# Optimization experiments

Measured on AMD Instinct MI355X. Metric: run time of the kernel, lower is better.

## Reference

```python
import jax, jax.numpy as jnp
import numpy as np


def gcn_conv(x, edge_index, edge_weight, W, b):
    """PyG-style GCNConv: h = x @ W; add self-loops (w=1); sym deg^-1/2 norm;
    scatter-add aggregation; + bias."""
    N = x.shape[0]
    h = x @ W                                   # [N, F_out]
    row, col = edge_index[0], edge_index[1]     # src, dst
    loop = jnp.arange(N)
    row = jnp.concatenate([row, loop])
    col = jnp.concatenate([col, loop])
    ew = jnp.concatenate([edge_weight, jnp.ones((N,), edge_weight.dtype)])
    deg = jax.ops.segment_sum(ew, col, num_segments=N)
    dinv = jnp.where(deg > 0, deg ** -0.5, 0.0)
    norm = dinv[row] * ew * dinv[col]           # [E+N]
    out = jax.ops.segment_sum(h[row] * norm[:, None], col, num_segments=N)
    return out + b


def setup_inputs() -> dict:
    key = jax.random.key(0)
    ks = jax.random.split(key, 12)
    N, F_in, H, O, E = 20000, 3000, 512, 256, 640000
    x = jax.random.normal(ks[0], (N, F_in), dtype=jnp.float32)
    sim_edge_index = jax.random.randint(ks[1], (2, E), 0, N, dtype=jnp.int64)
    sim_edge_weight = jax.random.uniform(ks[2], (E,), dtype=jnp.float32)
    dist_edge_index = jax.random.randint(ks[3], (2, E), 0, N, dtype=jnp.int64)
    dist_edge_weight = jax.random.uniform(ks[4], (E,), dtype=jnp.float32)
    s = 0.02
    return {
        "x": x,
        "sim_edge_index": sim_edge_index,
        "sim_edge_weight": sim_edge_weight,
        "dist_edge_index": dist_edge_index,
        "dist_edge_weight": dist_edge_weight,
        "W1": jax.random.normal(ks[5], (F_in, H), dtype=jnp.float32) * s,
        "b1": jnp.zeros((H,), jnp.float32),
        "W2": jax.random.normal(ks[6], (F_in, H), dtype=jnp.float32) * s,
        "b2": jnp.zeros((H,), jnp.float32),
        "Ws": jax.random.normal(ks[7], (H, O), dtype=jnp.float32) * s,
        "bs": jnp.zeros((O,), jnp.float32),
        "Wd": jax.random.normal(ks[8], (H, O), dtype=jnp.float32) * s,
        "bd": jnp.zeros((O,), jnp.float32),
        "Wf": jax.random.normal(ks[9], (2 * O, O), dtype=jnp.float32) * s,
        "bf": jnp.zeros((O,), jnp.float32),
    }


def reference(x, sim_edge_index, sim_edge_weight, dist_edge_index,
              dist_edge_weight, W1, b1, W2, b2, Ws, bs, Wd, bd, Wf, bf):
    # eval mode: dropout is identity
    xs = jax.nn.relu(gcn_conv(x, sim_edge_index, sim_edge_weight, W1, b1))
    xd = jax.nn.relu(gcn_conv(x, dist_edge_index, dist_edge_weight, W2, b2))
    x_sim = gcn_conv(xs, sim_edge_index, sim_edge_weight, Ws, bs)
    x_dist = gcn_conv(xd, dist_edge_index, dist_edge_weight, Wd, bd)
    fused = jnp.concatenate([x_sim, x_dist], axis=1) @ Wf + bf
    return (x_sim, x_dist, fused)
```

## Files before the change

kernel.cpp:

```cpp
#include <hip/hip_runtime.h>
#include <cstdint>
#include <cstddef>

typedef unsigned short u16;
typedef __bf16 bf16x8 __attribute__((ext_vector_type(8)));
typedef float f32x4 __attribute__((ext_vector_type(4)));

#define N_NODES 20000
#define MPAD    20096
#define E_EDGES 640000
#define K1      3000
#define K1P     3008
#define H_DIM   512
#define NW      1024
#define O_DIM   256

__device__ __forceinline__ float bf2f(unsigned int hi) {
  union { unsigned int u; float f; } v; v.u = hi << 16; return v.f;
}
__device__ __forceinline__ u16 f2bf(float f) {
  union { float f; unsigned int u; } v; v.f = f;
  unsigned int u = v.u;
  return (u16)((u + 0x7fffu + ((u >> 16) & 1u)) >> 16);
}

__device__ __forceinline__ void gl2lds16(const void* g, void* l) {
  __builtin_amdgcn_global_load_lds((const __attribute__((address_space(1))) void*)g,
                                   (__attribute__((address_space(3))) void*)l, 16, 0, 0);
}

__global__ __launch_bounds__(256) void deg_init_k(float* degS, float* degD, int* cntS, int* cntD) {
  int i = blockIdx.x * 256 + threadIdx.x;
  if (i < N_NODES) { degS[i] = 1.0f; degD[i] = 1.0f; cntS[i] = 0; cntD[i] = 0; }
}

__global__ __launch_bounds__(256) void deg_accum_k(const int* eiS, const float* ewS,
                                                   const int* eiD, const float* ewD,
                                                   float* degS, float* degD, int* cntS, int* cntD) {
  int e = blockIdx.x * 256 + threadIdx.x;
  if (e < E_EDGES) {
    int cs = eiS[E_EDGES + e];
    atomicAdd(&degS[cs], ewS[e]);
    atomicAdd(&cntS[cs], 1);
    int cd = eiD[E_EDGES + e];
    atomicAdd(&degD[cd], ewD[e]);
    atomicAdd(&cntD[cd], 1);
  }
}

__global__ __launch_bounds__(256) void dinv_k(const float* degS, const float* degD,
                                              float* dinvS, float* dinvD) {
  int i = blockIdx.x * 256 + threadIdx.x;
  if (i < N_NODES) { dinvS[i] = rsqrtf(degS[i]); dinvD[i] = rsqrtf(degD[i]); }
}

__global__ __launch_bounds__(1024) void scan_k(const int* cntS, int* offS, int* curS,
                                               const int* cntD, int* offD, int* curD) {
  const int* cnt = blockIdx.x ? cntD : cntS;
  int* off = blockIdx.x ? offD : offS;
  int* cur = blockIdx.x ? curD : curS;
  __shared__ int sums[1024];
  const int t = threadIdx.x;
  const int CH = 20;
  int base = t * CH;
  int s = 0;
  for (int j = 0; j < CH; ++j) { int idx = base + j; if (idx < N_NODES) s += cnt[idx]; }
  sums[t] = s;
  __syncthreads();
  for (int d = 1; d < 1024; d <<= 1) {
    int v = (t >= d) ? sums[t - d] : 0;
    __syncthreads();
    sums[t] += v;
    __syncthreads();
  }
  int run = sums[t] - s;
  for (int j = 0; j < CH; ++j) {
    int idx = base + j;
    if (idx <= N_NODES) {
      off[idx] = run; cur[idx] = run;
      if (idx < N_NODES) run += cnt[idx];
    }
  }
}

__global__ __launch_bounds__(256) void scatter_k(const int* eiS, const float* ewS, const float* dinvS,
                                                 int* curS, int* ssrcS, float* snrmS,
                                                 const int* eiD, const float* ewD, const float* dinvD,
                                                 int* curD, int* ssrcD, float* snrmD) {
  int e = blockIdx.x * 256 + threadIdx.x;
  if (e < E_EDGES) {
    {
      int r = eiS[e], c = eiS[E_EDGES + e];
      int pos = atomicAdd(&curS[c], 1);
      ssrcS[pos] = r;
      snrmS[pos] = dinvS[r] * ewS[e] * dinvS[c];
    }
    {
      int r = eiD[e], c = eiD[E_EDGES + e];
      int pos = atomicAdd(&curD[c], 1);
      ssrcD[pos] = r;
      snrmD[pos] = dinvD[r] * ewD[e] * dinvD[c];
    }
  }
}

__global__ __launch_bounds__(256) void conv_x_k(const float* __restrict__ x, u16* __restrict__ xb) {
  const int row = blockIdx.x;
  for (int c = threadIdx.x; c < 376; c += 256) {
    uint4 o = {0, 0, 0, 0};
    if (row < N_NODES && c < 375) {
      const float4* p = (const float4*)(x + (size_t)row * K1 + (size_t)c * 8);
      float4 v0 = p[0], v1 = p[1];
      o.x = f2bf(v0.x) | ((unsigned)f2bf(v0.y) << 16);
      o.y = f2bf(v0.z) | ((unsigned)f2bf(v0.w) << 16);
      o.z = f2bf(v1.x) | ((unsigned)f2bf(v1.y) << 16);
      o.w = f2bf(v1.z) | ((unsigned)f2bf(v1.w) << 16);
    }
    *(uint4*)(xb + (size_t)row * K1P + (size_t)c * 8) = o;
  }
}

__global__ __launch_bounds__(256) void conv_w12_k(const float* __restrict__ W1,
                                                  const float* __restrict__ W2,
                                                  u16* __restrict__ w12t) {
  __shared__ float t[64][65];
  const int kb = blockIdx.x;
  const int nb = blockIdx.y;
  const int n0 = nb * 64;
  const float* W = (n0 < H_DIM) ? W1 : W2;
  const int nn0 = n0 & (H_DIM - 1);
  const int k0 = kb * 64;
  const int tc = threadIdx.x & 63;
  const int tr4 = threadIdx.x >> 6;
#pragma unroll
  for (int rr = 0; rr < 16; ++rr) {
    int r = tr4 * 16 + rr;
    int k = k0 + r;
    t[r][tc] = (k < K1) ? W[(size_t)k * H_DIM + nn0 + tc] : 0.f;
  }
  __syncthreads();
#pragma unroll
  for (int rr = 0; rr < 16; ++rr) {
    int n = tr4 * 16 + rr;
    w12t[(size_t)(n0 + n) * K1P + k0 + tc] = f2bf(t[tc][n]);
  }
}

__global__ __launch_bounds__(256) void conv_wsm_k(const float* Ws, const float* Wd, const float* Wf,
                                                  u16* wst, u16* wdt, u16* wft) {
  __shared__ float t[64][65];
  const int which = blockIdx.z;
  const float* W = (which == 0) ? Ws : (which == 1) ? Wd : Wf;
  u16* o = (which == 0) ? wst : (which == 1) ? wdt : wft;
  const int k0 = blockIdx.x * 64;
  const int n0 = blockIdx.y * 64;
  const int tc = threadIdx.x & 63;
  const int tr4 = threadIdx.x >> 6;
#pragma unroll
  for (int rr = 0; rr < 16; ++rr) {
    int r = tr4 * 16 + rr;
    t[r][tc] = W[(size_t)(k0 + r) * O_DIM + n0 + tc];
  }
  __syncthreads();
#pragma unroll
  for (int rr = 0; rr < 16; ++rr) {
    int n = tr4 * 16 + rr;
    o[(size_t)(n0 + n) * H_DIM + k0 + tc] = f2bf(t[tc][n]);
  }
}

template <typename CT, bool BIAS>
__global__ __launch_bounds__(256) void gemm_bt(const u16* __restrict__ A, const u16* __restrict__ Bt,
                                               CT* __restrict__ C, const float* __restrict__ bias,
                                               int Mreal, int K, int ldc) {
  __shared__ alignas(16) u16 As[128 * 64];
  __shared__ alignas(16) u16 Bs[128 * 64];
  const int tid = threadIdx.x;
  const int lane = tid & 63;
  const int wv = tid >> 6;
  const int bm = blockIdx.y * 128;
  const int bn = blockIdx.x * 128;

  const int wm = (wv >> 1) << 6;
  const int wn = (wv & 1) << 6;
  const int frow = lane & 15;
  const int q = lane >> 4;
  const int r7 = lane & 7;

  const int srow = tid >> 3;
  const int sgr = ((tid & 7) ^ ((tid >> 3) & 7)) << 3;
  const u16* ga = A + (size_t)(bm + srow) * K + sgr;
  const u16* gb = Bt + (size_t)(bn + srow) * K + sgr;
  u16* la = &As[wv * 512];
  u16* lb = &Bs[wv * 512];

  f32x4 acc[4][4] = {};

  for (int k0 = 0; k0 < K; k0 += 64) {
#pragma unroll
    for (int r = 0; r < 4; ++r) {
      gl2lds16(ga + (size_t)(r * 32) * K + k0, la + r * 2048);
      gl2lds16(gb + (size_t)(r * 32) * K + k0, lb + r * 2048);
    }
    __syncthreads();
#pragma unroll
    for (int ks = 0; ks < 64; ks += 32) {
      const int p = (((q + (ks >> 3)) ^ r7) << 3);
      bf16x8 af[4], bv[4];
#pragma unroll
      for (int t = 0; t < 4; ++t) {
        af[t] = *(const bf16x8*)&As[(wm + t * 16 + frow) * 64 + p];
        bv[t] = *(const bf16x8*)&Bs[(wn + t * 16 + frow) * 64 + p];
      }
#pragma unroll
      for (int i = 0; i < 4; ++i)
#pragma unroll
        for (int j = 0; j < 4; ++j)
          acc[i][j] = __builtin_amdgcn_mfma_f32_16x16x32_bf16(af[i], bv[j], acc[i][j], 0, 0, 0);
    }
    __syncthreads();
  }

  const int crow = (lane >> 4) << 2;
  const int ccol = lane & 15;
#pragma unroll
  for (int i = 0; i < 4; ++i) {
#pragma unroll
    for (int r = 0; r < 4; ++r) {
      int gr = bm + wm + i * 16 + crow + r;
      if (gr < Mreal) {
#pragma unroll
        for (int j = 0; j < 4; ++j) {
          int gc = bn + wn + j * 16 + ccol;
          float v = acc[i][j][r];
          if constexpr (BIAS) v += bias[gc];
          if constexpr (sizeof(CT) == 2) C[(size_t)gr * ldc + gc] = (CT)f2bf(v);
          else C[(size_t)gr * ldc + gc] = (CT)v;
        }
      }
    }
  }
}

__global__ __launch_bounds__(256) void agg1_k(const u16* __restrict__ h12,
                                              const int* offS, const int* srcS, const float* nrmS,
                                              const float* dinvS, const float* b1,
                                              const int* offD, const int* srcD, const float* nrmD,
                                              const float* dinvD, const float* b2,
                                              u16* __restrict__ xsd) {
  const int lane = threadIdx.x & 63;
  const int wv = threadIdx.x >> 6;
  const int i = blockIdx.x * 4 + wv;
  const int g = blockIdx.y;
  if (i >= MPAD) return;
  u16* outp = xsd + ((size_t)g * MPAD + i) * H_DIM + lane * 8;
  if (i >= N_NODES) { uint4 z = {0, 0, 0, 0}; *(uint4*)outp = z; return; }

  const int* off = g ? offD : offS;
  const int* src = g ? srcD : srcS;
  const float* nrm = g ? nrmD : nrmS;
  const float* dinv = g ? dinvD : dinvS;
  const float* bias = g ? b2 : b1;
  const size_t cb = (size_t)g * H_DIM + lane * 8;

  float a[8];
  float dv = dinv[i];
  float sw = dv * dv;
  uint4 u = *(const uint4*)(h12 + (size_t)i * NW + cb);
  a[0] = sw * bf2f(u.x & 0xffff); a[1] = sw * bf2f(u.x >> 16);
  a[2] = sw * bf2f(u.y & 0xffff); a[3] = sw * bf2f(u.y >> 16);
  a[4] = sw * bf2f(u.z & 0xffff); a[5] = sw * bf2f(u.z >> 16);
  a[6] = sw * bf2f(u.w & 0xffff); a[7] = sw * bf2f(u.w >> 16);

  const int e0 = off[i], e1 = off[i + 1];
  for (int e = e0; e < e1; ++e) {
    int s = src[e];
    float w = nrm[e];
    uint4 v = *(const uint4*)(h12 + (size_t)s * NW + cb);
    a[0] += w * bf2f(v.x & 0xffff); a[1] += w * bf2f(v.x >> 16);
    a[2] += w * bf2f(v.y & 0xffff); a[3] += w * bf2f(v.y >> 16);
    a[4] += w * bf2f(v.z & 0xffff); a[5] += w * bf2f(v.z >> 16);
    a[6] += w * bf2f(v.w & 0xffff); a[7] += w * bf2f(v.w >> 16);
  }
  float4 bA = *(const float4*)(bias + lane * 8);
  float4 bB = *(const float4*)(bias + lane * 8 + 4);
  a[0] = fmaxf(a[0] + bA.x, 0.f); a[1] = fmaxf(a[1] + bA.y, 0.f);
  a[2] = fmaxf(a[2] + bA.z, 0.f); a[3] = fmaxf(a[3] + bA.w, 0.f);
  a[4] = fmaxf(a[4] + bB.x, 0.f); a[5] = fmaxf(a[5] + bB.y, 0.f);
  a[6] = fmaxf(a[6] + bB.z, 0.f); a[7] = fmaxf(a[7] + bB.w, 0.f);
  uint4 o;
  o.x = f2bf(a[0]) | ((unsigned)f2bf(a[1]) << 16);
  o.y = f2bf(a[2]) | ((unsigned)f2bf(a[3]) << 16);
  o.z = f2bf(a[4]) | ((unsigned)f2bf(a[5]) << 16);
  o.w = f2bf(a[6]) | ((unsigned)f2bf(a[7]) << 16);
  *(uint4*)outp = o;
}

__global__ __launch_bounds__(256) void agg2_k(const u16* __restrict__ hsb, const u16* __restrict__ hdb,
                                              const int* offS, const int* srcS, const float* nrmS,
                                              const float* dinvS, const float* bs,
                                              const int* offD, const int* srcD, const float* nrmD,
                                              const float* dinvD, const float* bd,
                                              float* __restrict__ outF, u16* __restrict__ xcat) {
  const int lane = threadIdx.x & 63;
  const int wv = threadIdx.x >> 6;
  const int i = blockIdx.x * 4 + wv;
  const int g = blockIdx.y;
  if (i >= MPAD) return;
  u16* oc = xcat + (size_t)i * H_DIM + (size_t)g * O_DIM + lane * 4;
  if (i >= N_NODES) { uint2 z = {0, 0}; *(uint2*)oc = z; return; }

  const u16* h = g ? hdb : hsb;
  const int* off = g ? offD : offS;
  const int* src = g ? srcD : srcS;
  const float* nrm = g ? nrmD : nrmS;
  const float* dinv = g ? dinvD : dinvS;
  const float* bias = g ? bd : bs;

  float a[4];
  float dv = dinv[i];
  float sw = dv * dv;
  uint2 u = *(const uint2*)(h + (size_t)i * O_DIM + lane * 4);
  a[0] = sw * bf2f(u.x & 0xffff); a[1] = sw * bf2f(u.x >> 16);
  a[2] = sw * bf2f(u.y & 0xffff); a[3] = sw * bf2f(u.y >> 16);

  const int e0 = off[i], e1 = off[i + 1];
  for (int e = e0; e < e1; ++e) {
    int s = src[e];
    float w = nrm[e];
    uint2 v = *(const uint2*)(h + (size_t)s * O_DIM + lane * 4);
    a[0] += w * bf2f(v.x & 0xffff); a[1] += w * bf2f(v.x >> 16);
    a[2] += w * bf2f(v.y & 0xffff); a[3] += w * bf2f(v.y >> 16);
  }
  float4 bb = *(const float4*)(bias + lane * 4);
  a[0] += bb.x; a[1] += bb.y; a[2] += bb.z; a[3] += bb.w;

  float4 fo = {a[0], a[1], a[2], a[3]};
  *(float4*)(outF + (size_t)g * N_NODES * O_DIM + (size_t)i * O_DIM + lane * 4) = fo;
  uint2 o;
  o.x = f2bf(a[0]) | ((unsigned)f2bf(a[1]) << 16);
  o.y = f2bf(a[2]) | ((unsigned)f2bf(a[3]) << 16);
  *(uint2*)oc = o;
}

extern "C" void kernel_launch(void* const* d_in, const int* in_sizes, int n_in,
                              void* d_out, int out_size, void* d_ws, size_t ws_size,
                              hipStream_t stream) {
  const float* x = (const float*)d_in[0];
  const int* eiS = (const int*)d_in[1];
  const float* ewS = (const float*)d_in[2];
  const int* eiD = (const int*)d_in[3];
  const float* ewD = (const float*)d_in[4];
  const float* W1 = (const float*)d_in[5];
  const float* b1 = (const float*)d_in[6];
  const float* W2 = (const float*)d_in[7];
  const float* b2 = (const float*)d_in[8];
  const float* Ws = (const float*)d_in[9];
  const float* bs = (const float*)d_in[10];
  const float* Wd = (const float*)d_in[11];
  const float* bd = (const float*)d_in[12];
  const float* Wf = (const float*)d_in[13];
  const float* bf_ = (const float*)d_in[14];
  float* out = (float*)d_out;

  char* p = (char*)d_ws;
  auto alloc = [&](size_t n) -> char* { char* r = p; p += (n + 255) & ~(size_t)255; return r; };

  u16* xb    = (u16*)alloc((size_t)MPAD * K1P * 2);
  u16* w12t  = (u16*)alloc((size_t)NW * K1P * 2);
  u16* h12   = (u16*)alloc((size_t)N_NODES * NW * 2);
  u16* xsd   = (u16*)alloc((size_t)2 * MPAD * H_DIM * 2);
  u16* hsb   = (u16*)alloc((size_t)N_NODES * O_DIM * 2);
  u16* hdb   = (u16*)alloc((size_t)N_NODES * O_DIM * 2);
  u16* xcat  = (u16*)alloc((size_t)MPAD * H_DIM * 2);
  u16* wst   = (u16*)alloc((size_t)O_DIM * H_DIM * 2);
  u16* wdt   = (u16*)alloc((size_t)O_DIM * H_DIM * 2);
  u16* wft   = (u16*)alloc((size_t)O_DIM * H_DIM * 2);
  float* degS = (float*)alloc((size_t)N_NODES * 4);
  float* degD = (float*)alloc((size_t)N_NODES * 4);
  float* dinvS = (float*)alloc((size_t)N_NODES * 4);
  float* dinvD = (float*)alloc((size_t)N_NODES * 4);
  int* cntS = (int*)alloc((size_t)N_NODES * 4);
  int* cntD = (int*)alloc((size_t)N_NODES * 4);
  int* offS = (int*)alloc((size_t)(N_NODES + 1) * 4);
  int* offD = (int*)alloc((size_t)(N_NODES + 1) * 4);
  int* curS = (int*)alloc((size_t)(N_NODES + 1) * 4);
  int* curD = (int*)alloc((size_t)(N_NODES + 1) * 4);
  int* ssrcS = (int*)alloc((size_t)E_EDGES * 4);
  int* ssrcD = (int*)alloc((size_t)E_EDGES * 4);
  float* snrmS = (float*)alloc((size_t)E_EDGES * 4);
  float* snrmD = (float*)alloc((size_t)E_EDGES * 4);

  const int gN = (N_NODES + 255) / 256;
  const int gE = (E_EDGES + 255) / 256;

  deg_init_k<<<gN, 256, 0, stream>>>(degS, degD, cntS, cntD);
  deg_accum_k<<<gE, 256, 0, stream>>>(eiS, ewS, eiD, ewD, degS, degD, cntS, cntD);
  dinv_k<<<gN, 256, 0, stream>>>(degS, degD, dinvS, dinvD);
  scan_k<<<2, 1024, 0, stream>>>(cntS, offS, curS, cntD, offD, curD);
  scatter_k<<<gE, 256, 0, stream>>>(eiS, ewS, dinvS, curS, ssrcS, snrmS,
                                    eiD, ewD, dinvD, curD, ssrcD, snrmD);

  conv_x_k<<<MPAD, 256, 0, stream>>>(x, xb);
  conv_w12_k<<<dim3(47, 16), 256, 0, stream>>>(W1, W2, w12t);
  conv_wsm_k<<<dim3(8, 4, 3), 256, 0, stream>>>(Ws, Wd, Wf, wst, wdt, wft);

  gemm_bt<u16, false><<<dim3(8, 157), 256, 0, stream>>>(xb, w12t, h12, nullptr, N_NODES, K1P, NW);

  agg1_k<<<dim3(MPAD / 4, 2), 256, 0, stream>>>(h12, offS, ssrcS, snrmS, dinvS, b1,
                                                offD, ssrcD, snrmD, dinvD, b2, xsd);

  gemm_bt<u16, false><<<dim3(2, 157), 256, 0, stream>>>(xsd, wst, hsb, nullptr, N_NODES, H_DIM, O_DIM);
  gemm_bt<u16, false><<<dim3(2, 157), 256, 0, stream>>>(xsd + (size_t)MPAD * H_DIM, wdt, hdb, nullptr,
                                                        N_NODES, H_DIM, O_DIM);

  agg2_k<<<dim3(MPAD / 4, 2), 256, 0, stream>>>(hsb, hdb, offS, ssrcS, snrmS, dinvS, bs,
                                                offD, ssrcD, snrmD, dinvD, bd, out, xcat);

  gemm_bt<float, true><<<dim3(2, 157), 256, 0, stream>>>(xcat, wft, out + (size_t)2 * N_NODES * O_DIM,
                                                         bf_, N_NODES, H_DIM, O_DIM);
}
```

Before: 1.134 ms.

## Split aggregation kernels into column chunks for cache-resident gather working sets

The two sparse aggregation kernels now give each block one 64-column chunk of the feature matrix, and a 16-lane group handles one node instead of a full wavefront covering all columns. Blocks in the x grid dimension (column chunk) run together, so the gathered feature slices for that chunk are meant to fit in L2/MALL and be reused across neighbouring nodes. Edge-index and weight loads and output stores are made nontemporal. The trade-off is that CSR indices and weights are re-read once per chunk (8x), and each gather moves only 8 bytes per lane, which cuts per-load efficiency.

```diff
diff --git a/kernel.cpp b/kernel.cpp
--- a/kernel.cpp
+++ b/kernel.cpp
@@ -5,6 +5,8 @@
 typedef unsigned short u16;
 typedef __bf16 bf16x8 __attribute__((ext_vector_type(8)));
 typedef float f32x4 __attribute__((ext_vector_type(4)));
+typedef unsigned int u32x2 __attribute__((ext_vector_type(2)));
+typedef float f32x4v __attribute__((ext_vector_type(4)));
 
 #define N_NODES 20000
 #define MPAD    20096
@@ -242,105 +244,100 @@
   }
 }
 
-__global__ __launch_bounds__(256) void agg1_k(const u16* __restrict__ h12,
-                                              const int* offS, const int* srcS, const float* nrmS,
-                                              const float* dinvS, const float* b1,
-                                              const int* offD, const int* srcD, const float* nrmD,
-                                              const float* dinvD, const float* b2,
-                                              u16* __restrict__ xsd) {
-  const int lane = threadIdx.x & 63;
-  const int wv = threadIdx.x >> 6;
-  const int i = blockIdx.x * 4 + wv;
-  const int g = blockIdx.y;
-  if (i >= MPAD) return;
-  u16* outp = xsd + ((size_t)g * MPAD + i) * H_DIM + lane * 8;
-  if (i >= N_NODES) { uint4 z = {0, 0, 0, 0}; *(uint4*)outp = z; return; }
-
-  const int* off = g ? offD : offS;
-  const int* src = g ? srcD : srcS;
-  const float* nrm = g ? nrmD : nrmS;
-  const float* dinv = g ? dinvD : dinvS;
-  const float* bias = g ? b2 : b1;
-  const size_t cb = (size_t)g * H_DIM + lane * 8;
-
-  float a[8];
+__global__ __launch_bounds__(256) void agg1_chunk_k(const u16* __restrict__ h12,
+                                                    const int* __restrict__ off,
+                                                    const int* __restrict__ src,
+                                                    const float* __restrict__ nrm,
+                                                    const float* __restrict__ dinv,
+                                                    const float* __restrict__ bias,
+                                                    u16* __restrict__ xsd_g, int gcol) {
+  const int c = blockIdx.x;
+  const int lane16 = threadIdx.x & 15;
+  const int sg = threadIdx.x >> 4;
+  const int i = blockIdx.y * 16 + sg;
+  const int col = c * 64 + lane16 * 4;
+  u32x2* outp = (u32x2*)(xsd_g + (size_t)i * H_DIM + col);
+  if (i >= N_NODES) {
+    u32x2 z = {0, 0};
+    __builtin_nontemporal_store(z, outp);
+    return;
+  }
+  const u16* base = h12 + (size_t)gcol + col;
+
   float dv = dinv[i];
   float sw = dv * dv;
-  uint4 u = *(const uint4*)(h12 + (size_t)i * NW + cb);
-  a[0] = sw * bf2f(u.x & 0xffff); a[1] = sw * bf2f(u.x >> 16);
-  a[2] = sw * bf2f(u.y & 0xffff); a[3] = sw * bf2f(u.y >> 16);
-  a[4] = sw * bf2f(u.z & 0xffff); a[5] = sw * bf2f(u.z >> 16);
-  a[6] = sw * bf2f(u.w & 0xffff); a[7] = sw * bf2f(u.w >> 16);
+  u32x2 u = *(const u32x2*)(base + (size_t)i * NW);
+  float a0 = sw * bf2f(u.x & 0xffff), a1 = sw * bf2f(u.x >> 16);
+  float a2 = sw * bf2f(u.y & 0xffff), a3 = sw * bf2f(u.y >> 16);
 
   const int e0 = off[i], e1 = off[i + 1];
   for (int e = e0; e < e1; ++e) {
-    int s = src[e];
-    float w = nrm[e];
-    uint4 v = *(const uint4*)(h12 + (size_t)s * NW + cb);
-    a[0] += w * bf2f(v.x & 0xffff); a[1] += w * bf2f(v.x >> 16);
-    a[2] += w * bf2f(v.y & 0xffff); a[3] += w * bf2f(v.y >> 16);
-    a[4] += w * bf2f(v.z & 0xffff); a[5] += w * bf2f(v.z >> 16);
-    a[6] += w * bf2f(v.w & 0xffff); a[7] += w * bf2f(v.w >> 16);
-  }
-  float4 bA = *(const float4*)(bias + lane * 8);
-  float4 bB = *(const float4*)(bias + lane * 8 + 4);
-  a[0] = fmaxf(a[0] + bA.x, 0.f); a[1] = fmaxf(a[1] + bA.y, 0.f);
-  a[2] = fmaxf(a[2] + bA.z, 0.f); a[3] = fmaxf(a[3] + bA.w, 0.f);
-  a[4] = fmaxf(a[4] + bB.x, 0.f); a[5] = fmaxf(a[5] + bB.y, 0.f);
-  a[6] = fmaxf(a[6] + bB.z, 0.f); a[7] = fmaxf(a[7] + bB.w, 0.f);
-  uint4 o;
-  o.x = f2bf(a[0]) | ((unsigned)f2bf(a[1]) << 16);
-  o.y = f2bf(a[2]) | ((unsigned)f2bf(a[3]) << 16);
-  o.z = f2bf(a[4]) | ((unsigned)f2bf(a[5]) << 16);
-  o.w = f2bf(a[6]) | ((unsigned)f2bf(a[7]) << 16);
-  *(uint4*)outp = o;
-}
-
-__global__ __launch_bounds__(256) void agg2_k(const u16* __restrict__ hsb, const u16* __restrict__ hdb,
-                                              const int* offS, const int* srcS, const float* nrmS,
-                                              const float* dinvS, const float* bs,
-                                              const int* offD, const int* srcD, const float* nrmD,
-                                              const float* dinvD, const float* bd,
-                                              float* __restrict__ outF, u16* __restrict__ xcat) {
-  const int lane = threadIdx.x & 63;
-  const int wv = threadIdx.x >> 6;
-  const int i = blockIdx.x * 4 + wv;
-  const int g = blockIdx.y;
-  if (i >= MPAD) return;
-  u16* oc = xcat + (size_t)i * H_DIM + (size_t)g * O_DIM + lane * 4;
-  if (i >= N_NODES) { uint2 z = {0, 0}; *(uint2*)oc = z; return; }
-
+    int s = __builtin_nontemporal_load(src + e);
+    float w = __builtin_nontemporal_load(nrm + e);
+    u32x2 v = *(const u32x2*)(base + (size_t)s * NW);
+    a0 += w * bf2f(v.x & 0xffff); a1 += w * bf2f(v.x >> 16);
+    a2 += w * bf2f(v.y & 0xffff); a3 += w * bf2f(v.y >> 16);
+  }
+  float4 bb = *(const float4*)(bias + col);
+  a0 = fmaxf(a0 + bb.x, 0.f); a1 = fmaxf(a1 + bb.y, 0.f);
+  a2 = fmaxf(a2 + bb.z, 0.f); a3 = fmaxf(a3 + bb.w, 0.f);
+  u32x2 o;
+  o.x = f2bf(a0) | ((unsigned)f2bf(a1) << 16);
+  o.y = f2bf(a2) | ((unsigned)f2bf(a3) << 16);
+  __builtin_nontemporal_store(o, outp);
+}
+
+__global__ __launch_bounds__(256) void agg2_chunk_k(const u16* __restrict__ hsb,
+                                                    const u16* __restrict__ hdb,
+                                                    const int* offS, const int* srcS, const float* nrmS,
+                                                    const float* dinvS, const float* bs,
+                                                    const int* offD, const int* srcD, const float* nrmD,
+                                                    const float* dinvD, const float* bd,
+                                                    float* __restrict__ outF, u16* __restrict__ xcat) {
+  const int cid = blockIdx.x;
+  const int g = cid >> 2;
+  const int c = cid & 3;
+  const int lane16 = threadIdx.x & 15;
+  const int sg = threadIdx.x >> 4;
+  const int i = blockIdx.y * 16 + sg;
+  const int col = c * 64 + lane16 * 4;
+  u32x2* oc = (u32x2*)(xcat + (size_t)i * H_DIM + (size_t)g * O_DIM + col);
+  if (i >= N_NODES) {
+    u32x2 z = {0, 0};
+    __builtin_nontemporal_store(z, oc);
+    return;
+  }
   const u16* h = g ? hdb : hsb;
   const int* off = g ? offD : offS;
   const int* src = g ? srcD : srcS;
   const float* nrm = g ? nrmD : nrmS;
   const float* dinv = g ? dinvD : dinvS;
   const float* bias = g ? bd : bs;
-
-  float a[4];
+  const u16* base = h + col;
+
   float dv = dinv[i];
   float sw = dv * dv;
-  uint2 u = *(const uint2*)(h + (size_t)i * O_DIM + lane * 4);
-  a[0] = sw * bf2f(u.x & 0xffff); a[1] = sw * bf2f(u.x >> 16);
-  a[2] = sw * bf2f(u.y & 0xffff); a[3] = sw * bf2f(u.y >> 16);
+  u32x2 u = *(const u32x2*)(base + (size_t)i * O_DIM);
+  float a0 = sw * bf2f(u.x & 0xffff), a1 = sw * bf2f(u.x >> 16);
+  float a2 = sw * bf2f(u.y & 0xffff), a3 = sw * bf2f(u.y >> 16);
 
   const int e0 = off[i], e1 = off[i + 1];
   for (int e = e0; e < e1; ++e) {
-    int s = src[e];
-    float w = nrm[e];
-    uint2 v = *(const uint2*)(h + (size_t)s * O_DIM + lane * 4);
-    a[0] += w * bf2f(v.x & 0xffff); a[1] += w * bf2f(v.x >> 16);
-    a[2] += w * bf2f(v.y & 0xffff); a[3] += w * bf2f(v.y >> 16);
-  }
-  float4 bb = *(const float4*)(bias + lane * 4);
-  a[0] += bb.x; a[1] += bb.y; a[2] += bb.z; a[3] += bb.w;
-
-  float4 fo = {a[0], a[1], a[2], a[3]};
-  *(float4*)(outF + (size_t)g * N_NODES * O_DIM + (size_t)i * O_DIM + lane * 4) = fo;
-  uint2 o;
-  o.x = f2bf(a[0]) | ((unsigned)f2bf(a[1]) << 16);
-  o.y = f2bf(a[2]) | ((unsigned)f2bf(a[3]) << 16);
-  *(uint2*)oc = o;
+    int s = __builtin_nontemporal_load(src + e);
+    float w = __builtin_nontemporal_load(nrm + e);
+    u32x2 v = *(const u32x2*)(base + (size_t)s * O_DIM);
+    a0 += w * bf2f(v.x & 0xffff); a1 += w * bf2f(v.x >> 16);
+    a2 += w * bf2f(v.y & 0xffff); a3 += w * bf2f(v.y >> 16);
+  }
+  float4 bb = *(const float4*)(bias + col);
+  a0 += bb.x; a1 += bb.y; a2 += bb.z; a3 += bb.w;
+
+  f32x4v fo = {a0, a1, a2, a3};
+  __builtin_nontemporal_store(fo, (f32x4v*)(outF + (size_t)g * N_NODES * O_DIM + (size_t)i * O_DIM + col));
+  u32x2 o;
+  o.x = f2bf(a0) | ((unsigned)f2bf(a1) << 16);
+  o.y = f2bf(a2) | ((unsigned)f2bf(a3) << 16);
+  __builtin_nontemporal_store(o, oc);
 }
 
 extern "C" void kernel_launch(void* const* d_in, const int* in_sizes, int n_in,
@@ -407,15 +404,18 @@
 
   gemm_bt<u16, false><<<dim3(8, 157), 256, 0, stream>>>(xb, w12t, h12, nullptr, N_NODES, K1P, NW);
 
-  agg1_k<<<dim3(MPAD / 4, 2), 256, 0, stream>>>(h12, offS, ssrcS, snrmS, dinvS, b1,
-                                                offD, ssrcD, snrmD, dinvD, b2, xsd);
+  agg1_chunk_k<<<dim3(8, MPAD / 16), 256, 0, stream>>>(h12, offS, ssrcS, snrmS, dinvS, b1,
+                                                       xsd, 0);
+  agg1_chunk_k<<<dim3(8, MPAD / 16), 256, 0, stream>>>(h12, offD, ssrcD, snrmD, dinvD, b2,
+                                                       xsd + (size_t)MPAD * H_DIM, H_DIM);
 
   gemm_bt<u16, false><<<dim3(2, 157), 256, 0, stream>>>(xsd, wst, hsb, nullptr, N_NODES, H_DIM, O_DIM);
   gemm_bt<u16, false><<<dim3(2, 157), 256, 0, stream>>>(xsd + (size_t)MPAD * H_DIM, wdt, hdb, nullptr,
                                                         N_NODES, H_DIM, O_DIM);
 
-  agg2_k<<<dim3(MPAD / 4, 2), 256, 0, stream>>>(hsb, hdb, offS, ssrcS, snrmS, dinvS, bs,
-                                                offD, ssrcD, snrmD, dinvD, bd, out, xcat);
+  agg2_chunk_k<<<dim3(8, MPAD / 16), 256, 0, stream>>>(hsb, hdb,
+                                                       offS, ssrcS, snrmS, dinvS, bs,
+                                                       offD, ssrcD, snrmD, dinvD, bd, out, xcat);
 
   gemm_bt<float, true><<<dim3(2, 157), 256, 0, stream>>>(xcat, wft, out + (size_t)2 * N_NODES * O_DIM,
                                                          bf_, N_NODES, H_DIM, O_DIM);
```

After: 1.554 ms. 1.37x slower.
